# Performance work log

Measured on AMD Instinct MI355X. Metric: run time of the kernel, lower is better.

## Reference

```python
import jax, jax.numpy as jnp
import numpy as np

B, J, I, N = 128, 32, 1152, 16
SPARSE_TOPK = [0.3, 0.3]  # parsed from '0.3;0.3'


def squash(s, axis=-1):
    # v = (|s|^2 / (1 + |s|^2)) * s / |s|
    sq = jnp.sum(s * s, axis=axis, keepdims=True)
    return (sq / (1.0 + sq)) * s / jnp.sqrt(sq)


def setup_inputs() -> dict:
    key = jax.random.key(0)
    u_hat = jax.random.normal(key, (B, J, I, N), dtype=jnp.float32)
    # bias_routing=True -> Parameter(zeros(j,n)).fill_(0.1)
    bias = jnp.full((J, N), 0.1, dtype=jnp.float32)
    return {"u_hat": u_hat, "bias": bias, "iters": 3}


def reference(u_hat, bias, iters):
    b = u_hat.shape[0]
    b_vec = jnp.zeros((b, J, I), dtype=u_hat.dtype)
    stats = []
    v_vec = None
    for index in range(iters):
        # routing coefficients: softmax over output capsules j
        c_vec = jax.nn.softmax(b_vec, axis=1)  # [b,j,i]
        # entropy over dim=1, mean over remaining dims (calc_entropy(...).mean())
        c_safe = jnp.where(c_vec > 0, c_vec, 1.0)
        ent = -jnp.sum(c_vec * jnp.log(c_safe), axis=1)  # [b,i]
        stats.append(jnp.mean(ent))
        # s_vec = (c_vec[b,j,1,i] @ u_hat[b,j,i,n]).squeeze()
        s_vec = jnp.einsum('bji,bjin->bjn', c_vec, u_hat)
        # bias + reset of all-zero rows
        s_vec_bias = s_vec + bias
        reset_mask = (jnp.sum(s_vec, axis=2) == 0)[..., None]  # [b,j,1]
        s_vec_bias = jnp.where(reset_mask, 0.0, s_vec_bias)
        v_vec = squash(s_vec_bias)  # [b,j,n]
        if index < iters - 1:
            # agreement update: u_hat[b,j,i,1,n] @ v_vec[b,j,1,n,1] -> [b,j,i]
            b_vec = b_vec + jnp.einsum('bjin,bjn->bji', u_hat, v_vec)
            # sparsify_edges_topk: mask bottom-k along j per (b,i) column
            mask_count = int(SPARSE_TOPK[index] * J)
            if mask_count > 0:
                # kth smallest along j == max of bottom-k (-inf sorts first, as in torch.topk smallest)
                kth = jnp.sort(b_vec, axis=1)[:, mask_count - 1:mask_count, :]  # [b,1,i]
                b_vec = jnp.where(b_vec <= kth, -jnp.inf, b_vec)
    return v_vec, jnp.stack(stats)
```

## Files before the change

### kernel.cpp

```cpp
#include <hip/hip_runtime.h>
#include <math.h>


#define NB 128
#define NJ 32
#define NI 1152
#define NN 16
#define TI 32
#define NTILES (NI / TI)
#define COLS_TOTAL (NB * NI)

__device__ __forceinline__ int bca(int j, int col) {
  return j * 33 + ((col + 4 * j) & 31);
}

__global__ __launch_bounds__(256) void k_reduce_s0(const float* __restrict__ u,
                                                   float* __restrict__ s0) {
  int bj = blockIdx.x;
  const float4* u4 = (const float4*)u + (size_t)bj * (NI * NN / 4);
  int t = threadIdx.x;
  float4 acc = make_float4(0.f, 0.f, 0.f, 0.f);
#pragma unroll
  for (int k = 0; k < 18; ++k) {
    float4 x = u4[t + 256 * k];
    acc.x += x.x; acc.y += x.y; acc.z += x.z; acc.w += x.w;
  }
#pragma unroll
  for (int m = 4; m <= 32; m <<= 1) {
    acc.x += __shfl_xor(acc.x, m);
    acc.y += __shfl_xor(acc.y, m);
    acc.z += __shfl_xor(acc.z, m);
    acc.w += __shfl_xor(acc.w, m);
  }
  __shared__ float4 parts[4][4];
  int lane = t & 63, w = t >> 6;
  if (lane < 4) parts[w][lane] = acc;
  __syncthreads();
  if (t < 4) {
    float4 p0 = parts[0][t], p1 = parts[1][t], p2 = parts[2][t], p3 = parts[3][t];
    float4 r;
    r.x = (p0.x + p1.x + p2.x + p3.x) * (1.0f / 32.0f);
    r.y = (p0.y + p1.y + p2.y + p3.y) * (1.0f / 32.0f);
    r.z = (p0.z + p1.z + p2.z + p3.z) * (1.0f / 32.0f);
    r.w = (p0.w + p1.w + p2.w + p3.w) * (1.0f / 32.0f);
    ((float4*)(s0 + (size_t)bj * NN))[t] = r;
  }
}

__global__ __launch_bounds__(256) void k_squash(const float* __restrict__ s,
                                                const float* __restrict__ bias,
                                                float* __restrict__ vout,
                                                const float* __restrict__ ent,
                                                int write_stats) {
  int gid = blockIdx.x * 256 + threadIdx.x;
  int n = gid & 15;
  int j = (gid >> 4) & 31;
  float sv = s[gid];
  float ssum = sv;
#pragma unroll
  for (int m = 1; m < 16; m <<= 1) ssum += __shfl_xor(ssum, m);
  float sb = sv + bias[j * NN + n];
  if (ssum == 0.0f) sb = 0.0f;
  float sq = sb * sb;
#pragma unroll
  for (int m = 1; m < 16; m <<= 1) sq += __shfl_xor(sq, m);
  vout[gid] = (sq / (1.0f + sq)) * sb / sqrtf(sq);
  if (write_stats && gid < 3) {
    float val = (gid == 0) ? logf(32.0f) : ent[gid - 1] / (float)COLS_TOTAL;
    vout[NB * NJ * NN + gid] = val;
  }
}

template <int SPARS>
__global__ __launch_bounds__(256) void k_route(const float* __restrict__ u,
                                               const float* __restrict__ vprev,
                                               const float* __restrict__ v0,
                                               float* __restrict__ kth0,
                                               float* __restrict__ s_out,
                                               float* __restrict__ ent_accum) {
  __shared__ float bc[32 * 33];
  __shared__ float ct[32 * 33];
  __shared__ float entc[32];

  int t = threadIdx.x;
  int bid = blockIdx.x;
  int b = bid / NTILES;
  int tile = bid - b * NTILES;
  int i0 = tile * TI;
  int j = t >> 3, cg = t & 7;

  const float4* up = (const float4*)u + ((size_t)(b * NJ + j) * NI + i0 + cg) * 4;
  float4 Ur[4][4];
#pragma unroll
  for (int k = 0; k < 4; ++k)
#pragma unroll
    for (int q = 0; q < 4; ++q) Ur[k][q] = up[k * 32 + q];

  float kthc[4];
  if (SPARS == 0) {
#pragma unroll
    for (int k = 0; k < 4; ++k) kthc[k] = kth0[b * NI + i0 + cg + 8 * k];
  }
  const float4* vA4 = (const float4*)vprev + (b * NJ + j) * 4;
  const float4* vB4 = (const float4*)v0 + (b * NJ + j) * 4;
  float accA[4] = {0.f, 0.f, 0.f, 0.f};
  float accB[4] = {0.f, 0.f, 0.f, 0.f};
#pragma unroll
  for (int q = 0; q < 4; ++q) {
    float4 vaq = vA4[q];
    float4 vbq;
    if (SPARS == 0) vbq = vB4[q];
#pragma unroll
    for (int k = 0; k < 4; ++k) {
      float4 uu = Ur[k][q];
      accA[k] = fmaf(uu.x, vaq.x, accA[k]);
      accA[k] = fmaf(uu.y, vaq.y, accA[k]);
      accA[k] = fmaf(uu.z, vaq.z, accA[k]);
      accA[k] = fmaf(uu.w, vaq.w, accA[k]);
      if (SPARS == 0) {
        accB[k] = fmaf(uu.x, vbq.x, accB[k]);
        accB[k] = fmaf(uu.y, vbq.y, accB[k]);
        accB[k] = fmaf(uu.z, vbq.z, accB[k]);
        accB[k] = fmaf(uu.w, vbq.w, accB[k]);
      }
    }
  }
#pragma unroll
  for (int k = 0; k < 4; ++k) {
    float bv;
    if (SPARS)
      bv = accA[k];
    else
      bv = ((accB[k] <= kthc[k]) ? -INFINITY : accB[k]) + accA[k];
    bc[bca(j, cg + 8 * k)] = bv;
  }
  __syncthreads();

  {
    int col = t >> 3, sg = t & 7;
    float own0 = bc[bca(sg * 4 + 0, col)];
    float own1 = bc[bca(sg * 4 + 1, col)];
    float own2 = bc[bca(sg * 4 + 2, col)];
    float own3 = bc[bca(sg * 4 + 3, col)];
    float m;
    if (SPARS) {
      int r0 = 0, r1 = 0, r2 = 0, r3 = 0, e0 = 0, e1 = 0, e2 = 0, e3 = 0;
      m = -INFINITY;
#pragma unroll
      for (int jj = 0; jj < 32; ++jj) {
        float bj = bc[bca(jj, col)];
        m = fmaxf(m, bj);
        r0 += (bj < own0); e0 += (bj == own0);
        r1 += (bj < own1); e1 += (bj == own1);
        r2 += (bj < own2); e2 += (bj == own2);
        r3 += (bj < own3); e3 += (bj == own3);
      }
      float cand = -INFINITY;
      if (r0 <= 8 && 8 < r0 + e0) cand = fmaxf(cand, own0);
      if (r1 <= 8 && 8 < r1 + e1) cand = fmaxf(cand, own1);
      if (r2 <= 8 && 8 < r2 + e2) cand = fmaxf(cand, own2);
      if (r3 <= 8 && 8 < r3 + e3) cand = fmaxf(cand, own3);
      cand = fmaxf(cand, __shfl_xor(cand, 1));
      cand = fmaxf(cand, __shfl_xor(cand, 2));
      cand = fmaxf(cand, __shfl_xor(cand, 4));
      if (own0 <= cand) own0 = -INFINITY;
      if (own1 <= cand) own1 = -INFINITY;
      if (own2 <= cand) own2 = -INFINITY;
      if (own3 <= cand) own3 = -INFINITY;
      if (sg == 0) kth0[b * NI + i0 + col] = cand;
    } else {
      float lm = fmaxf(fmaxf(own0, own1), fmaxf(own2, own3));
      lm = fmaxf(lm, __shfl_xor(lm, 1));
      lm = fmaxf(lm, __shfl_xor(lm, 2));
      lm = fmaxf(lm, __shfl_xor(lm, 4));
      m = lm;
    }
    float x0 = expf(own0 - m), x1 = expf(own1 - m);
    float x2 = expf(own2 - m), x3 = expf(own3 - m);
    float ps = (x0 + x1) + (x2 + x3);
    ps += __shfl_xor(ps, 1);
    ps += __shfl_xor(ps, 2);
    ps += __shfl_xor(ps, 4);
    float c0 = x0 / ps, c1 = x1 / ps, c2 = x2 / ps, c3 = x3 / ps;
    ct[bca(sg * 4 + 0, col)] = c0;
    ct[bca(sg * 4 + 1, col)] = c1;
    ct[bca(sg * 4 + 2, col)] = c2;
    ct[bca(sg * 4 + 3, col)] = c3;
    float ent = 0.f;
    if (c0 > 0.f) ent += c0 * logf(c0);
    if (c1 > 0.f) ent += c1 * logf(c1);
    if (c2 > 0.f) ent += c2 * logf(c2);
    if (c3 > 0.f) ent += c3 * logf(c3);
    ent += __shfl_xor(ent, 1);
    ent += __shfl_xor(ent, 2);
    ent += __shfl_xor(ent, 4);
    if (sg == 0) entc[col] = -ent;
  }
  __syncthreads();

  {
    float part[16];
#pragma unroll
    for (int n = 0; n < 16; ++n) part[n] = 0.f;
#pragma unroll
    for (int k = 0; k < 4; ++k) {
      float c = ct[bca(j, cg + 8 * k)];
#pragma unroll
      for (int q = 0; q < 4; ++q) {
        float4 uu = Ur[k][q];
        part[4 * q + 0] = fmaf(c, uu.x, part[4 * q + 0]);
        part[4 * q + 1] = fmaf(c, uu.y, part[4 * q + 1]);
        part[4 * q + 2] = fmaf(c, uu.z, part[4 * q + 2]);
        part[4 * q + 3] = fmaf(c, uu.w, part[4 * q + 3]);
      }
    }
    float nw[8];
#pragma unroll
    for (int i = 0; i < 8; ++i) {
      float send = (cg & 1) ? part[i] : part[i + 8];
      float recv = __shfl_xor(send, 1);
      nw[i] = ((cg & 1) ? part[i + 8] : part[i]) + recv;
    }
    float n2[4];
#pragma unroll
    for (int i = 0; i < 4; ++i) {
      float send = (cg & 2) ? nw[i] : nw[i + 4];
      float recv = __shfl_xor(send, 2);
      n2[i] = ((cg & 2) ? nw[i + 4] : nw[i]) + recv;
    }
    float n3[2];
#pragma unroll
    for (int i = 0; i < 2; ++i) {
      float send = (cg & 4) ? n2[i] : n2[i + 2];
      float recv = __shfl_xor(send, 4);
      n3[i] = ((cg & 4) ? n2[i + 2] : n2[i]) + recv;
    }
    int base = (cg & 1) * 8 + (cg & 2) * 2 + ((cg & 4) >> 1);
    int outi = (b * NJ + j) * NN + base;
    unsafeAtomicAdd(&s_out[outi], n3[0]);
    unsafeAtomicAdd(&s_out[outi + 1], n3[1]);
  }
  if (t < 32) {
    float e = entc[t];
    e += __shfl_xor(e, 1);
    e += __shfl_xor(e, 2);
    e += __shfl_xor(e, 4);
    e += __shfl_xor(e, 8);
    e += __shfl_xor(e, 16);
    if (t == 0) unsafeAtomicAdd(ent_accum, e);
  }
}

extern "C" void kernel_launch(void* const* d_in, const int* in_sizes, int n_in,
                              void* d_out, int out_size, void* d_ws, size_t ws_size,
                              hipStream_t stream) {
  (void)in_sizes; (void)n_in; (void)out_size; (void)ws_size;
  const float* u = (const float*)d_in[0];
  const float* bias = (const float*)d_in[1];
  float* ws = (float*)d_ws;
  float* s1 = ws;
  float* s2 = ws + 65536;
  float* ent = ws + 131072;
  float* s0 = ws + 131076;
  float* v0 = ws + 196612;
  float* v1 = ws + 262148;
  float* kth0 = ws + 327684;
  float* dout = (float*)d_out;

  hipMemsetAsync(d_ws, 0, (size_t)(131072 + 4) * sizeof(float), stream);

  k_reduce_s0<<<dim3(NB * NJ), dim3(256), 0, stream>>>(u, s0);
  k_squash<<<dim3(256), dim3(256), 0, stream>>>(s0, bias, v0, (const float*)nullptr, 0);
  k_route<1><<<dim3(NB * NTILES), dim3(256), 0, stream>>>(u, v0, v0, kth0, s1, ent + 0);
  k_squash<<<dim3(256), dim3(256), 0, stream>>>(s1, bias, v1, (const float*)nullptr, 0);
  k_route<0><<<dim3(NB * NTILES), dim3(256), 0, stream>>>(u, v1, v0, kth0, s2, ent + 1);
  k_squash<<<dim3(256), dim3(256), 0, stream>>>(s2, bias, dout, ent, 1);
}
```

Baseline: 573.1 us.

## Fuse squash into routing kernels and reverse block order for cache reuse

Removes the two intermediate squash kernel launches by recomputing the squash of the per-batch s vectors inside each routing block into shared memory. The first routing kernel also walks blocks in reverse order, so the second pass starts on the u_hat tiles touched most recently and may hit them in cache. The cost is redundant squash work in every block (36 tiles per batch recompute the same 512 values) plus an extra barrier.

```diff
diff --git a/kernel.cpp b/kernel.cpp
--- a/kernel.cpp
+++ b/kernel.cpp
@@ -8,10 +8,30 @@
 #define NN 16
 #define TI 32
 #define NTILES (NI / TI)
+#define NBLK (NB * NTILES)
 #define COLS_TOTAL (NB * NI)
 
 __device__ __forceinline__ int bca(int j, int col) {
   return j * 33 + ((col + 4 * j) & 31);
+}
+
+__device__ __forceinline__ void inline_squash(const float* __restrict__ s,
+                                              const float* __restrict__ bias,
+                                              int b, float* vsh, int t) {
+#pragma unroll
+  for (int p = 0; p < 2; ++p) {
+    int idx = p * 256 + t;
+    float sv = s[b * 512 + idx];
+    float ssum = sv;
+#pragma unroll
+    for (int m = 1; m < 16; m <<= 1) ssum += __shfl_xor(ssum, m);
+    float sb = sv + bias[idx];
+    if (ssum == 0.0f) sb = 0.0f;
+    float sq = sb * sb;
+#pragma unroll
+    for (int m = 1; m < 16; m <<= 1) sq += __shfl_xor(sq, m);
+    vsh[(idx >> 4) * 20 + (idx & 15)] = (sq / (1.0f + sq)) * sb / sqrtf(sq);
+  }
 }
 
 __global__ __launch_bounds__(256) void k_reduce_s0(const float* __restrict__ u,
@@ -47,11 +67,10 @@
   }
 }
 
-__global__ __launch_bounds__(256) void k_squash(const float* __restrict__ s,
-                                                const float* __restrict__ bias,
-                                                float* __restrict__ vout,
-                                                const float* __restrict__ ent,
-                                                int write_stats) {
+__global__ __launch_bounds__(256) void k_final(const float* __restrict__ s,
+                                               const float* __restrict__ bias,
+                                               float* __restrict__ vout,
+                                               const float* __restrict__ ent) {
   int gid = blockIdx.x * 256 + threadIdx.x;
   int n = gid & 15;
   int j = (gid >> 4) & 31;
@@ -65,25 +84,28 @@
 #pragma unroll
   for (int m = 1; m < 16; m <<= 1) sq += __shfl_xor(sq, m);
   vout[gid] = (sq / (1.0f + sq)) * sb / sqrtf(sq);
-  if (write_stats && gid < 3) {
+  if (gid < 3) {
     float val = (gid == 0) ? logf(32.0f) : ent[gid - 1] / (float)COLS_TOTAL;
     vout[NB * NJ * NN + gid] = val;
   }
 }
 
-template <int SPARS>
+template <int SPARS, int REV>
 __global__ __launch_bounds__(256) void k_route(const float* __restrict__ u,
-                                               const float* __restrict__ vprev,
-                                               const float* __restrict__ v0,
+                                               const float* __restrict__ sA,
+                                               const float* __restrict__ sB,
+                                               const float* __restrict__ bias,
                                                float* __restrict__ kth0,
                                                float* __restrict__ s_out,
                                                float* __restrict__ ent_accum) {
+  __shared__ __align__(16) float vAsh[NJ * 20];
+  __shared__ __align__(16) float vBsh[NJ * 20];
   __shared__ float bc[32 * 33];
   __shared__ float ct[32 * 33];
   __shared__ float entc[32];
 
   int t = threadIdx.x;
-  int bid = blockIdx.x;
+  int bid = REV ? (NBLK - 1 - (int)blockIdx.x) : (int)blockIdx.x;
   int b = bid / NTILES;
   int tile = bid - b * NTILES;
   int i0 = tile * TI;
@@ -96,20 +118,23 @@
 #pragma unroll
     for (int q = 0; q < 4; ++q) Ur[k][q] = up[k * 32 + q];
 
+  inline_squash(sA, bias, b, vAsh, t);
+  if (SPARS == 0) inline_squash(sB, bias, b, vBsh, t);
+
   float kthc[4];
   if (SPARS == 0) {
 #pragma unroll
     for (int k = 0; k < 4; ++k) kthc[k] = kth0[b * NI + i0 + cg + 8 * k];
   }
-  const float4* vA4 = (const float4*)vprev + (b * NJ + j) * 4;
-  const float4* vB4 = (const float4*)v0 + (b * NJ + j) * 4;
+  __syncthreads();
+
   float accA[4] = {0.f, 0.f, 0.f, 0.f};
   float accB[4] = {0.f, 0.f, 0.f, 0.f};
 #pragma unroll
   for (int q = 0; q < 4; ++q) {
-    float4 vaq = vA4[q];
+    float4 vaq = *(const float4*)&vAsh[j * 20 + q * 4];
     float4 vbq;
-    if (SPARS == 0) vbq = vB4[q];
+    if (SPARS == 0) vbq = *(const float4*)&vBsh[j * 20 + q * 4];
 #pragma unroll
     for (int k = 0; k < 4; ++k) {
       float4 uu = Ur[k][q];
@@ -262,17 +287,13 @@
   float* s2 = ws + 65536;
   float* ent = ws + 131072;
   float* s0 = ws + 131076;
-  float* v0 = ws + 196612;
-  float* v1 = ws + 262148;
-  float* kth0 = ws + 327684;
+  float* kth0 = ws + 196612;
   float* dout = (float*)d_out;
 
   hipMemsetAsync(d_ws, 0, (size_t)(131072 + 4) * sizeof(float), stream);
 
   k_reduce_s0<<<dim3(NB * NJ), dim3(256), 0, stream>>>(u, s0);
-  k_squash<<<dim3(256), dim3(256), 0, stream>>>(s0, bias, v0, (const float*)nullptr, 0);
-  k_route<1><<<dim3(NB * NTILES), dim3(256), 0, stream>>>(u, v0, v0, kth0, s1, ent + 0);
-  k_squash<<<dim3(256), dim3(256), 0, stream>>>(s1, bias, v1, (const float*)nullptr, 0);
-  k_route<0><<<dim3(NB * NTILES), dim3(256), 0, stream>>>(u, v1, v0, kth0, s2, ent + 1);
-  k_squash<<<dim3(256), dim3(256), 0, stream>>>(s2, bias, dout, ent, 1);
-}
+  k_route<1, 1><<<dim3(NBLK), dim3(256), 0, stream>>>(u, s0, s0, bias, kth0, s1, ent + 0);
+  k_route<0, 0><<<dim3(NBLK), dim3(256), 0, stream>>>(u, s1, s0, bias, kth0, s2, ent + 1);
+  k_final<<<dim3(256), dim3(256), 0, stream>>>(s2, bias, dout, ent);
+}
```

After: 568.4 us. Within noise of the previous version (-0.8%).
